# Performance work log

Measured on AMD Instinct MI355X. Metric: run time of the kernel, lower is better.

The kernel has to match this reference:

```python
import jax, jax.numpy as jnp
import numpy as np

N = 50000        # nodes
E = 800000       # edges
D_IN = 64        # input_dim
D_E = 16         # edge_dim
D_OUT = 64       # output_dim
HEADS = 8
HEAD_DIM = D_OUT // HEADS
COMB = 2 * D_IN + D_E  # 144


def _linear_init(key, fan_in, fan_out):
    kw, kb = jax.random.split(key)
    lim = 1.0 / np.sqrt(fan_in)
    W = jax.random.uniform(kw, (fan_in, fan_out), minval=-lim, maxval=lim, dtype=jnp.float32)
    b = jax.random.uniform(kb, (fan_out,), minval=-lim, maxval=lim, dtype=jnp.float32)
    return W, b


def setup_inputs() -> dict:
    key = jax.random.key(0)
    ks = jax.random.split(key, 16)
    inp = {
        "x": jax.random.normal(ks[0], (N, D_IN), dtype=jnp.float32),
        "edge_attr": jax.random.normal(ks[1], (E, D_E), dtype=jnp.float32),
        "edge_index": jax.random.randint(ks[2], (2, E), 0, N, dtype=jnp.int32),
        "q": jax.random.uniform(ks[3], (1, D_OUT), dtype=jnp.float32) * 0.1,
    }
    # three ResidualStacks: k (COMB->D_OUT), v (COMB->D_OUT), out (D_OUT->D_OUT)
    for pre, fan_in, kbase in (("k", COMB, 4), ("v", COMB, 8), ("o", D_OUT, 12)):
        W0, b0 = _linear_init(ks[kbase], fan_in, D_OUT)
        W1, b1 = _linear_init(ks[kbase + 1], D_OUT, D_OUT)
        W2, b2 = _linear_init(ks[kbase + 2], D_OUT, D_OUT)
        inp.update({f"{pre}_W0": W0, f"{pre}_b0": b0,
                    f"{pre}_W1": W1, f"{pre}_b1": b1,
                    f"{pre}_W2": W2, f"{pre}_b2": b2})
    return inp


def residual_stack(h, W0, b0, W1, b1, W2, b2, last_activation):
    # input projection + ReLU, then 2 residual linear blocks
    h = jax.nn.relu(h @ W0 + b0)
    h = jax.nn.relu(h + h @ W1 + b1)
    h = h + h @ W2 + b2
    if last_activation:
        h = jax.nn.relu(h)
    return h


def neighborhood_attention(q, k, v, index):
    # q: (1, D_OUT), k/v: (E, D_OUT), index: (E,) destination node ids
    kh = k.reshape(E, HEADS, HEAD_DIM)
    qh = q.reshape(1, HEADS, HEAD_DIM)
    scores = jnp.sum(qh * kh, axis=-1) / np.sqrt(HEAD_DIM)  # (E, HEADS)
    m = jax.ops.segment_max(scores, index, num_segments=N)  # (N, HEADS)
    ex = jnp.exp(scores - jax.lax.stop_gradient(m)[index])
    denom = jax.ops.segment_sum(ex, index, num_segments=N)  # (N, HEADS)
    alpha = ex / denom[index]
    vh = v.reshape(E, HEADS, HEAD_DIM)
    return (alpha[:, :, None] * vh).reshape(E, D_OUT)


def reference(x, edge_attr, edge_index, q,
              k_W0, k_b0, k_W1, k_b1, k_W2, k_b2,
              v_W0, v_b0, v_W1, v_b1, v_W2, v_b2,
              o_W0, o_b0, o_W1, o_b1, o_W2, o_b2):
    src, dst = edge_index[0], edge_index[1]
    feat = jnp.concatenate([x[src], x[dst], edge_attr], axis=-1)  # (E, COMB)
    k = residual_stack(feat, k_W0, k_b0, k_W1, k_b1, k_W2, k_b2, last_activation=False)
    v = residual_stack(feat, v_W0, v_b0, v_W1, v_b1, v_W2, v_b2, last_activation=False)
    messages = neighborhood_attention(q, k, v, dst)               # (E, D_OUT)
    aggr = jax.ops.segment_sum(messages, dst, num_segments=N)    # (N, D_OUT)
    out = residual_stack(jax.nn.relu(aggr), o_W0, o_b0, o_W1, o_b1, o_W2, o_b2, last_activation=False)
    # skip_connection=True, input_dim == output_dim -> identity skip
    return jax.nn.relu(x + out)
```

## Files before the change

### kernel.cpp

```cpp
#include <hip/hip_runtime.h>

#define N_NODES 50000
#define E_EDGES 800000
#define D_OUT   64
#define COMB    144

typedef float  f32x4  __attribute__((ext_vector_type(4)));
typedef __bf16 bf16x8 __attribute__((ext_vector_type(8)));
typedef __bf16 bf16x4 __attribute__((ext_vector_type(4)));

#define WS_NUM_OFF   0
#define WS_DEN_OFF   (12800000)
#define WS_WTS_OFF   (14400000)
#define BIG_ELEMS    (64*168)
#define SMALL_ELEMS  (64*72)

__global__ __launch_bounds__(256) void prep_kernel(
    const float* __restrict__ kW0, const float* __restrict__ kW1, const float* __restrict__ kW2,
    const float* __restrict__ vW0, const float* __restrict__ vW1, const float* __restrict__ vW2,
    const float* __restrict__ oW0, const float* __restrict__ oW1, const float* __restrict__ oW2,
    __bf16* __restrict__ wout)
{
    const int b = blockIdx.x, tid = threadIdx.x;
    const float* src;
    __bf16* dst;
    int K, Kpad, lb;
    if (b < 42)      { src = kW0; dst = wout;             K = 144; Kpad = 168; lb = b; }
    else if (b < 84) { src = vW0; dst = wout + BIG_ELEMS; K = 144; Kpad = 168; lb = b - 42; }
    else {
        const int id = (b - 84) / 18; lb = (b - 84) % 18;
        const float* s7[7] = {kW1, kW2, vW1, vW2, oW0, oW1, oW2};
        src = s7[id]; dst = wout + 2 * BIG_ELEMS + id * SMALL_ELEMS;
        K = 64; Kpad = 72;
    }
    const int idx = lb * 256 + tid;
    const int col = idx / Kpad, k = idx % Kpad;
    dst[idx] = (k < K) ? (__bf16)src[k * 64 + col] : (__bf16)0.f;
}

__device__ __forceinline__ void gemm64(const __bf16* Arow, const __bf16* Wt,
                                       int hi, int row16, f32x4 acc[4])
{
    #pragma unroll
    for (int kc = 0; kc < 2; ++kc) {
        const bf16x8 a = *(const bf16x8*)(Arow + kc * 32 + hi * 8);
        #pragma unroll
        for (int n = 0; n < 4; ++n) {
            const bf16x8 bfr = *(const bf16x8*)(Wt + (n * 16 + row16) * 72 + kc * 32 + hi * 8);
            acc[n] = __builtin_amdgcn_mfma_f32_16x16x32_bf16(a, bfr, acc[n], 0, 0, 0);
        }
    }
}

__global__ __launch_bounds__(256) void edge_kernel(
    const float* __restrict__ x,
    const float* __restrict__ edge_attr,
    const int*   __restrict__ edge_index,
    const float* __restrict__ q,
    const float* __restrict__ kb0, const float* __restrict__ kb1, const float* __restrict__ kb2,
    const float* __restrict__ vb0, const float* __restrict__ vb1, const float* __restrict__ vb2,
    const __bf16* __restrict__ kW0t, const __bf16* __restrict__ kW1t, const __bf16* __restrict__ kW2t,
    const __bf16* __restrict__ vW0t, const __bf16* __restrict__ vW1t, const __bf16* __restrict__ vW2t,
    float* __restrict__ num, float* __restrict__ den)
{
    __shared__ __bf16 feat_s[64][168];
    __shared__ __bf16 H0_s[64][72];
    __shared__ __bf16 H1_s[64][72];
    __shared__ int src_s[64], dst_s[64];

    const int tid  = threadIdx.x;
    const int lane = tid & 63;
    const int w    = tid >> 6;
    const int e0   = blockIdx.x * 64;
    const int row16 = lane & 15;
    const int hi    = lane >> 4;

    if (tid < 64) { src_s[tid] = edge_index[e0 + tid]; dst_s[tid] = edge_index[E_EDGES + e0 + tid]; }
    __syncthreads();

    for (int i = tid; i < 64 * 36; i += 256) {
        const int r = i / 36, j = i % 36;
        float4 f;
        if (j < 16)      f = *(const float4*)&x[(size_t)src_s[r] * 64 + j * 4];
        else if (j < 32) f = *(const float4*)&x[(size_t)dst_s[r] * 64 + (j - 16) * 4];
        else             f = *(const float4*)&edge_attr[(size_t)(e0 + r) * 16 + (j - 32) * 4];
        bf16x4 h; h[0] = (__bf16)f.x; h[1] = (__bf16)f.y; h[2] = (__bf16)f.z; h[3] = (__bf16)f.w;
        *(bf16x4*)&feat_s[r][j * 4] = h;
    }
    for (int i = tid; i < 64 * 6; i += 256) {
        bf16x4 z; z[0] = z[1] = z[2] = z[3] = (__bf16)0.f;
        *(bf16x4*)&feat_s[i / 6][144 + (i % 6) * 4] = z;
    }
    __syncthreads();

    const __bf16* frow = &feat_s[w * 16 + row16][0];
    const __bf16* hrow0 = &H0_s[w * 16 + row16][0];
    const __bf16* hrow1 = &H1_s[w * 16 + row16][0];

    float kk[4][4], vv[4][4];

    #pragma unroll
    for (int stack = 0; stack < 2; ++stack) {
        const __bf16* W0t = stack == 0 ? kW0t : vW0t;
        const __bf16* W1t = stack == 0 ? kW1t : vW1t;
        const __bf16* W2t = stack == 0 ? kW2t : vW2t;
        const float*  b0  = stack == 0 ? kb0 : vb0;
        const float*  b1  = stack == 0 ? kb1 : vb1;
        const float*  b2  = stack == 0 ? kb2 : vb2;

        f32x4 acc[4] = {{0,0,0,0},{0,0,0,0},{0,0,0,0},{0,0,0,0}};
        #pragma unroll
        for (int kc = 0; kc < 5; ++kc) {
            const bf16x8 a = *(const bf16x8*)(frow + kc * 32 + hi * 8);
            #pragma unroll
            for (int n = 0; n < 4; ++n) {
                const bf16x8 bfr = *(const bf16x8*)(W0t + (n * 16 + row16) * 168 + kc * 32 + hi * 8);
                acc[n] = __builtin_amdgcn_mfma_f32_16x16x32_bf16(a, bfr, acc[n], 0, 0, 0);
            }
        }
        float h0[4][4];
        #pragma unroll
        for (int n = 0; n < 4; ++n) {
            const float bias = b0[n * 16 + row16];
            #pragma unroll
            for (int r = 0; r < 4; ++r) {
                h0[n][r] = fmaxf(acc[n][r] + bias, 0.f);
                H0_s[w * 16 + hi * 4 + r][n * 16 + row16] = (__bf16)h0[n][r];
            }
        }

        f32x4 acc1[4] = {{0,0,0,0},{0,0,0,0},{0,0,0,0},{0,0,0,0}};
        gemm64(hrow0, W1t, hi, row16, acc1);
        float h1[4][4];
        #pragma unroll
        for (int n = 0; n < 4; ++n) {
            const float bias = b1[n * 16 + row16];
            #pragma unroll
            for (int r = 0; r < 4; ++r) {
                h1[n][r] = fmaxf(h0[n][r] + acc1[n][r] + bias, 0.f);
                H1_s[w * 16 + hi * 4 + r][n * 16 + row16] = (__bf16)h1[n][r];
            }
        }

        f32x4 acc2[4] = {{0,0,0,0},{0,0,0,0},{0,0,0,0},{0,0,0,0}};
        gemm64(hrow1, W2t, hi, row16, acc2);
        #pragma unroll
        for (int n = 0; n < 4; ++n) {
            const float bias = b2[n * 16 + row16];
            #pragma unroll
            for (int r = 0; r < 4; ++r) {
                const float o = h1[n][r] + acc2[n][r] + bias;
                if (stack == 0) kk[n][r] = o; else vv[n][r] = o;
            }
        }
    }

    float qv[4];
    #pragma unroll
    for (int n = 0; n < 4; ++n) qv[n] = q[n * 16 + row16];

    float ex[4][4];
    #pragma unroll
    for (int n = 0; n < 4; ++n)
        #pragma unroll
        for (int r = 0; r < 4; ++r) {
            float p = qv[n] * kk[n][r];
            p += __shfl_xor(p, 1);
            p += __shfl_xor(p, 2);
            p += __shfl_xor(p, 4);
            ex[n][r] = __expf(p * 0.35355339059327373f);
        }

    const int b3 = row16 >> 3;
    #pragma unroll
    for (int r = 0; r < 4; ++r) {
        const int drow = dst_s[w * 16 + hi * 4 + r];
        if ((lane & 7) == 0) {
            #pragma unroll
            for (int n = 0; n < 4; ++n)
                atomicAdd(&den[(size_t)drow * 8 + 2 * n + b3], ex[n][r]);
        }
        #pragma unroll
        for (int n = 0; n < 4; ++n)
            atomicAdd(&num[(size_t)drow * 64 + n * 16 + row16], ex[n][r] * vv[n][r]);
    }
}

__global__ __launch_bounds__(256) void node_kernel(
    const float* __restrict__ x,
    const float* __restrict__ num, const float* __restrict__ den,
    const float* __restrict__ ob0, const float* __restrict__ ob1, const float* __restrict__ ob2,
    const __bf16* __restrict__ oW0t, const __bf16* __restrict__ oW1t, const __bf16* __restrict__ oW2t,
    float* __restrict__ out)
{
    __shared__ __bf16 A_s[64][72];
    __shared__ __bf16 H0_s[64][72];
    __shared__ __bf16 H1_s[64][72];

    const int tid  = threadIdx.x;
    const int lane = tid & 63;
    const int w    = tid >> 6;
    const int n0   = blockIdx.x * 64;
    const int row16 = lane & 15;
    const int hi    = lane >> 4;

    for (int i = tid; i < 64 * 16; i += 256) {
        const int r = i >> 4, c4 = (i & 15) * 4;
        const int node = n0 + r;
        bf16x4 h; h[0] = h[1] = h[2] = h[3] = (__bf16)0.f;
        if (node < N_NODES) {
            const float dh = den[(size_t)node * 8 + (c4 >> 3)];
            if (dh > 0.f) {
                const float4 f = *(const float4*)&num[(size_t)node * 64 + c4];
                const float inv = 1.f / dh;
                h[0] = (__bf16)fmaxf(f.x * inv, 0.f);
                h[1] = (__bf16)fmaxf(f.y * inv, 0.f);
                h[2] = (__bf16)fmaxf(f.z * inv, 0.f);
                h[3] = (__bf16)fmaxf(f.w * inv, 0.f);
            }
        }
        *(bf16x4*)&A_s[r][c4] = h;
    }
    __syncthreads();

    const __bf16* arow  = &A_s[w * 16 + row16][0];
    const __bf16* hrow0 = &H0_s[w * 16 + row16][0];
    const __bf16* hrow1 = &H1_s[w * 16 + row16][0];

    f32x4 acc[4] = {{0,0,0,0},{0,0,0,0},{0,0,0,0},{0,0,0,0}};
    gemm64(arow, oW0t, hi, row16, acc);
    float h0[4][4];
    #pragma unroll
    for (int n = 0; n < 4; ++n) {
        const float bias = ob0[n * 16 + row16];
        #pragma unroll
        for (int r = 0; r < 4; ++r) {
            h0[n][r] = fmaxf(acc[n][r] + bias, 0.f);
            H0_s[w * 16 + hi * 4 + r][n * 16 + row16] = (__bf16)h0[n][r];
        }
    }

    f32x4 acc1[4] = {{0,0,0,0},{0,0,0,0},{0,0,0,0},{0,0,0,0}};
    gemm64(hrow0, oW1t, hi, row16, acc1);
    float h1[4][4];
    #pragma unroll
    for (int n = 0; n < 4; ++n) {
        const float bias = ob1[n * 16 + row16];
        #pragma unroll
        for (int r = 0; r < 4; ++r) {
            h1[n][r] = fmaxf(h0[n][r] + acc1[n][r] + bias, 0.f);
            H1_s[w * 16 + hi * 4 + r][n * 16 + row16] = (__bf16)h1[n][r];
        }
    }

    f32x4 acc2[4] = {{0,0,0,0},{0,0,0,0},{0,0,0,0},{0,0,0,0}};
    gemm64(hrow1, oW2t, hi, row16, acc2);
    #pragma unroll
    for (int n = 0; n < 4; ++n) {
        const float bias = ob2[n * 16 + row16];
        #pragma unroll
        for (int r = 0; r < 4; ++r) {
            const int node = n0 + w * 16 + hi * 4 + r;
            if (node < N_NODES) {
                const int col = n * 16 + row16;
                const float o = h1[n][r] + acc2[n][r] + bias;
                out[(size_t)node * 64 + col] = fmaxf(x[(size_t)node * 64 + col] + o, 0.f);
            }
        }
    }
}

extern "C" void kernel_launch(void* const* d_in, const int* in_sizes, int n_in,
                              void* d_out, int out_size, void* d_ws, size_t ws_size,
                              hipStream_t stream) {
    const float* x  = (const float*)d_in[0];
    const float* ea = (const float*)d_in[1];
    const int*   ei = (const int*)d_in[2];
    const float* q  = (const float*)d_in[3];
    const float* kW0 = (const float*)d_in[4];  const float* kb0 = (const float*)d_in[5];
    const float* kW1 = (const float*)d_in[6];  const float* kb1 = (const float*)d_in[7];
    const float* kW2 = (const float*)d_in[8];  const float* kb2 = (const float*)d_in[9];
    const float* vW0 = (const float*)d_in[10]; const float* vb0 = (const float*)d_in[11];
    const float* vW1 = (const float*)d_in[12]; const float* vb1 = (const float*)d_in[13];
    const float* vW2 = (const float*)d_in[14]; const float* vb2 = (const float*)d_in[15];
    const float* oW0 = (const float*)d_in[16]; const float* ob0 = (const float*)d_in[17];
    const float* oW1 = (const float*)d_in[18]; const float* ob1 = (const float*)d_in[19];
    const float* oW2 = (const float*)d_in[20]; const float* ob2 = (const float*)d_in[21];

    char* ws = (char*)d_ws;
    float*  num  = (float*)(ws + WS_NUM_OFF);
    float*  den  = (float*)(ws + WS_DEN_OFF);
    __bf16* wts  = (__bf16*)(ws + WS_WTS_OFF);
    __bf16* kW0t = wts;
    __bf16* vW0t = wts + BIG_ELEMS;
    __bf16* sm   = wts + 2 * BIG_ELEMS;
    __bf16* kW1t = sm;                  __bf16* kW2t = sm + SMALL_ELEMS;
    __bf16* vW1t = sm + 2 * SMALL_ELEMS; __bf16* vW2t = sm + 3 * SMALL_ELEMS;
    __bf16* oW0t = sm + 4 * SMALL_ELEMS; __bf16* oW1t = sm + 5 * SMALL_ELEMS;
    __bf16* oW2t = sm + 6 * SMALL_ELEMS;

    hipMemsetAsync(d_ws, 0, (size_t)N_NODES * (64 + 8) * sizeof(float), stream);

    prep_kernel<<<210, 256, 0, stream>>>(kW0, kW1, kW2, vW0, vW1, vW2, oW0, oW1, oW2, wts);

    edge_kernel<<<E_EDGES / 64, 256, 0, stream>>>(
        x, ea, ei, q,
        kb0, kb1, kb2, vb0, vb1, vb2,
        kW0t, kW1t, kW2t, vW0t, vW1t, vW2t,
        num, den);

    node_kernel<<<(N_NODES + 63) / 64, 256, 0, stream>>>(
        x, num, den, ob0, ob1, ob2, oW0t, oW1t, oW2t, (float*)d_out);
}
```

Baseline: 560.1 us.

## Make edge kernel persistent with register-prefetched gathers for next tile

The edge kernel now launches a fixed grid of 1024 blocks that loop over edge tiles with a grid stride. While the current tile's K/V MLPs run, each thread gathers the next tile's x rows and edge attributes into registers, and double-buffers the src/dst indices in shared memory. The aim is to hide gather latency behind the MFMA work and to cut block launch and setup overhead. The H0/H1 shared buffers are merged into one, and `__launch_bounds__(256,4)` caps registers, which adds pressure and a risk of spills alongside the extra prefetch registers.

```diff
diff --git a/kernel.cpp b/kernel.cpp
--- a/kernel.cpp
+++ b/kernel.cpp
@@ -4,6 +4,7 @@
 #define E_EDGES 800000
 #define D_OUT   64
 #define COMB    144
+#define GRID_E  1024
 
 typedef float  f32x4  __attribute__((ext_vector_type(4)));
 typedef __bf16 bf16x8 __attribute__((ext_vector_type(8)));
@@ -52,7 +53,7 @@
     }
 }
 
-__global__ __launch_bounds__(256) void edge_kernel(
+__global__ __launch_bounds__(256, 4) void edge_kernel(
     const float* __restrict__ x,
     const float* __restrict__ edge_attr,
     const int*   __restrict__ edge_index,
@@ -64,125 +65,226 @@
     float* __restrict__ num, float* __restrict__ den)
 {
     __shared__ __bf16 feat_s[64][168];
-    __shared__ __bf16 H0_s[64][72];
-    __shared__ __bf16 H1_s[64][72];
-    __shared__ int src_s[64], dst_s[64];
-
-    const int tid  = threadIdx.x;
-    const int lane = tid & 63;
-    const int w    = tid >> 6;
-    const int e0   = blockIdx.x * 64;
+    __shared__ __bf16 H_s[64][72];
+    __shared__ int    idx_s[2][128];
+
+    const int tid   = threadIdx.x;
+    const int lane  = tid & 63;
+    const int w     = tid >> 6;
     const int row16 = lane & 15;
     const int hi    = lane >> 4;
-
-    if (tid < 64) { src_s[tid] = edge_index[e0 + tid]; dst_s[tid] = edge_index[E_EDGES + e0 + tid]; }
-    __syncthreads();
-
-    for (int i = tid; i < 64 * 36; i += 256) {
-        const int r = i / 36, j = i % 36;
-        float4 f;
-        if (j < 16)      f = *(const float4*)&x[(size_t)src_s[r] * 64 + j * 4];
-        else if (j < 32) f = *(const float4*)&x[(size_t)dst_s[r] * 64 + (j - 16) * 4];
-        else             f = *(const float4*)&edge_attr[(size_t)(e0 + r) * 16 + (j - 32) * 4];
-        bf16x4 h; h[0] = (__bf16)f.x; h[1] = (__bf16)f.y; h[2] = (__bf16)f.z; h[3] = (__bf16)f.w;
-        *(bf16x4*)&feat_s[r][j * 4] = h;
-    }
+    const int wrow  = w * 16;
+
+    const int jj  = tid & 31;
+    const int rb  = tid >> 5;
+    const int sel = (jj < 16) ? 0 : 64;
+    const int c4  = (jj & 15) * 4;
+
+    const int nt = E_EDGES / 64;
+
     for (int i = tid; i < 64 * 6; i += 256) {
         bf16x4 z; z[0] = z[1] = z[2] = z[3] = (__bf16)0.f;
         *(bf16x4*)&feat_s[i / 6][144 + (i % 6) * 4] = z;
     }
+
+    float qv4[4];
+    #pragma unroll
+    for (int n = 0; n < 4; ++n) qv4[n] = q[n * 16 + row16];
+
+    int t = blockIdx.x;
+    if (tid < 128)
+        idx_s[0][tid] = edge_index[(tid >= 64 ? E_EDGES + t * 64 + tid - 64
+                                              : t * 64 + tid)];
     __syncthreads();
-
-    const __bf16* frow = &feat_s[w * 16 + row16][0];
-    const __bf16* hrow0 = &H0_s[w * 16 + row16][0];
-    const __bf16* hrow1 = &H1_s[w * 16 + row16][0];
-
-    float kk[4][4], vv[4][4];
-
-    #pragma unroll
-    for (int stack = 0; stack < 2; ++stack) {
-        const __bf16* W0t = stack == 0 ? kW0t : vW0t;
-        const __bf16* W1t = stack == 0 ? kW1t : vW1t;
-        const __bf16* W2t = stack == 0 ? kW2t : vW2t;
-        const float*  b0  = stack == 0 ? kb0 : vb0;
-        const float*  b1  = stack == 0 ? kb1 : vb1;
-        const float*  b2  = stack == 0 ? kb2 : vb2;
-
-        f32x4 acc[4] = {{0,0,0,0},{0,0,0,0},{0,0,0,0},{0,0,0,0}};
-        #pragma unroll
-        for (int kc = 0; kc < 5; ++kc) {
-            const bf16x8 a = *(const bf16x8*)(frow + kc * 32 + hi * 8);
-            #pragma unroll
-            for (int n = 0; n < 4; ++n) {
-                const bf16x8 bfr = *(const bf16x8*)(W0t + (n * 16 + row16) * 168 + kc * 32 + hi * 8);
-                acc[n] = __builtin_amdgcn_mfma_f32_16x16x32_bf16(a, bfr, acc[n], 0, 0, 0);
-            }
-        }
-        float h0[4][4];
-        #pragma unroll
-        for (int n = 0; n < 4; ++n) {
-            const float bias = b0[n * 16 + row16];
+    {
+        float4 g[8];
+        #pragma unroll
+        for (int k = 0; k < 8; ++k) {
+            const int node = idx_s[0][sel + rb + k * 8];
+            g[k] = *(const float4*)&x[(size_t)node * 64 + c4];
+        }
+        const float4 ea4 = *(const float4*)&edge_attr[((size_t)t * 64 + (tid >> 2)) * 16 + (tid & 3) * 4];
+        #pragma unroll
+        for (int k = 0; k < 8; ++k) {
+            bf16x4 h; h[0] = (__bf16)g[k].x; h[1] = (__bf16)g[k].y;
+                      h[2] = (__bf16)g[k].z; h[3] = (__bf16)g[k].w;
+            *(bf16x4*)&feat_s[rb + k * 8][sel + c4] = h;
+        }
+        bf16x4 he; he[0] = (__bf16)ea4.x; he[1] = (__bf16)ea4.y;
+                   he[2] = (__bf16)ea4.z; he[3] = (__bf16)ea4.w;
+        *(bf16x4*)&feat_s[tid >> 2][128 + (tid & 3) * 4] = he;
+
+        if (t + GRID_E < nt && tid < 128)
+            idx_s[1][tid] = edge_index[(tid >= 64 ? E_EDGES + (t + GRID_E) * 64 + tid - 64
+                                                  : (t + GRID_E) * 64 + tid)];
+    }
+    __syncthreads();
+
+    int bufA = 0;
+
+    for (; t < nt; t += GRID_E) {
+        const int  B    = bufA ^ 1;
+        const bool pre  = (t + GRID_E)     < nt;
+        const bool pre2 = (t + 2 * GRID_E) < nt;
+
+        float4 g[8]; float4 ea4;
+        if (pre) {
+            #pragma unroll
+            for (int k = 0; k < 8; ++k) {
+                const int node = idx_s[B][sel + rb + k * 8];
+                g[k] = *(const float4*)&x[(size_t)node * 64 + c4];
+            }
+            ea4 = *(const float4*)&edge_attr[((size_t)(t + GRID_E) * 64 + (tid >> 2)) * 16 + (tid & 3) * 4];
+        }
+        int inext = 0;
+        if (pre2 && tid < 128)
+            inext = edge_index[(tid >= 64 ? E_EDGES + (t + 2 * GRID_E) * 64 + tid - 64
+                                          : (t + 2 * GRID_E) * 64 + tid)];
+
+        const __bf16* frow = &feat_s[wrow + row16][0];
+        const __bf16* hrow = &H_s[wrow + row16][0];
+
+        float kk[4][4], vv[4][4];
+        float h0V[4][4];
+
+        {
+            f32x4 acc[4] = {{0,0,0,0},{0,0,0,0},{0,0,0,0},{0,0,0,0}};
+            #pragma unroll
+            for (int kc = 0; kc < 5; ++kc) {
+                const bf16x8 a = *(const bf16x8*)(frow + kc * 32 + hi * 8);
+                #pragma unroll
+                for (int n = 0; n < 4; ++n) {
+                    const bf16x8 bfr = *(const bf16x8*)(kW0t + (n * 16 + row16) * 168 + kc * 32 + hi * 8);
+                    acc[n] = __builtin_amdgcn_mfma_f32_16x16x32_bf16(a, bfr, acc[n], 0, 0, 0);
+                }
+            }
+            float h0[4][4];
+            #pragma unroll
+            for (int n = 0; n < 4; ++n) {
+                const float bias = kb0[n * 16 + row16];
+                #pragma unroll
+                for (int r = 0; r < 4; ++r) {
+                    h0[n][r] = fmaxf(acc[n][r] + bias, 0.f);
+                    H_s[wrow + hi * 4 + r][n * 16 + row16] = (__bf16)h0[n][r];
+                }
+            }
+            f32x4 acc1[4] = {{0,0,0,0},{0,0,0,0},{0,0,0,0},{0,0,0,0}};
+            gemm64(hrow, kW1t, hi, row16, acc1);
+            float h1[4][4];
+            #pragma unroll
+            for (int n = 0; n < 4; ++n) {
+                const float bias = kb1[n * 16 + row16];
+                #pragma unroll
+                for (int r = 0; r < 4; ++r) {
+                    h1[n][r] = fmaxf(h0[n][r] + acc1[n][r] + bias, 0.f);
+                    H_s[wrow + hi * 4 + r][n * 16 + row16] = (__bf16)h1[n][r];
+                }
+            }
+            f32x4 acc2[4] = {{0,0,0,0},{0,0,0,0},{0,0,0,0},{0,0,0,0}};
+            gemm64(hrow, kW2t, hi, row16, acc2);
+            #pragma unroll
+            for (int n = 0; n < 4; ++n) {
+                const float bias = kb2[n * 16 + row16];
+                #pragma unroll
+                for (int r = 0; r < 4; ++r)
+                    kk[n][r] = h1[n][r] + acc2[n][r] + bias;
+            }
+        }
+
+        float ex[4][4];
+        #pragma unroll
+        for (int n = 0; n < 4; ++n)
             #pragma unroll
             for (int r = 0; r < 4; ++r) {
-                h0[n][r] = fmaxf(acc[n][r] + bias, 0.f);
-                H0_s[w * 16 + hi * 4 + r][n * 16 + row16] = (__bf16)h0[n][r];
-            }
-        }
-
-        f32x4 acc1[4] = {{0,0,0,0},{0,0,0,0},{0,0,0,0},{0,0,0,0}};
-        gemm64(hrow0, W1t, hi, row16, acc1);
-        float h1[4][4];
-        #pragma unroll
-        for (int n = 0; n < 4; ++n) {
-            const float bias = b1[n * 16 + row16];
-            #pragma unroll
-            for (int r = 0; r < 4; ++r) {
-                h1[n][r] = fmaxf(h0[n][r] + acc1[n][r] + bias, 0.f);
-                H1_s[w * 16 + hi * 4 + r][n * 16 + row16] = (__bf16)h1[n][r];
-            }
-        }
-
-        f32x4 acc2[4] = {{0,0,0,0},{0,0,0,0},{0,0,0,0},{0,0,0,0}};
-        gemm64(hrow1, W2t, hi, row16, acc2);
-        #pragma unroll
-        for (int n = 0; n < 4; ++n) {
-            const float bias = b2[n * 16 + row16];
-            #pragma unroll
-            for (int r = 0; r < 4; ++r) {
-                const float o = h1[n][r] + acc2[n][r] + bias;
-                if (stack == 0) kk[n][r] = o; else vv[n][r] = o;
-            }
-        }
-    }
-
-    float qv[4];
-    #pragma unroll
-    for (int n = 0; n < 4; ++n) qv[n] = q[n * 16 + row16];
-
-    float ex[4][4];
-    #pragma unroll
-    for (int n = 0; n < 4; ++n)
+                float p = qv4[n] * kk[n][r];
+                p += __shfl_xor(p, 1);
+                p += __shfl_xor(p, 2);
+                p += __shfl_xor(p, 4);
+                ex[n][r] = __expf(p * 0.35355339059327373f);
+            }
+
+        int dst4[4];
+        #pragma unroll
+        for (int r = 0; r < 4; ++r) dst4[r] = idx_s[bufA][64 + wrow + hi * 4 + r];
+
+        {
+            f32x4 acc[4] = {{0,0,0,0},{0,0,0,0},{0,0,0,0},{0,0,0,0}};
+            #pragma unroll
+            for (int kc = 0; kc < 5; ++kc) {
+                const bf16x8 a = *(const bf16x8*)(frow + kc * 32 + hi * 8);
+                #pragma unroll
+                for (int n = 0; n < 4; ++n) {
+                    const bf16x8 bfr = *(const bf16x8*)(vW0t + (n * 16 + row16) * 168 + kc * 32 + hi * 8);
+                    acc[n] = __builtin_amdgcn_mfma_f32_16x16x32_bf16(a, bfr, acc[n], 0, 0, 0);
+                }
+            }
+            #pragma unroll
+            for (int n = 0; n < 4; ++n) {
+                const float bias = vb0[n * 16 + row16];
+                #pragma unroll
+                for (int r = 0; r < 4; ++r) {
+                    h0V[n][r] = fmaxf(acc[n][r] + bias, 0.f);
+                    H_s[wrow + hi * 4 + r][n * 16 + row16] = (__bf16)h0V[n][r];
+                }
+            }
+        }
+
+        __syncthreads();
+
+        if (pre2 && tid < 128) idx_s[bufA][tid] = inext;
+
+        {
+            f32x4 acc1[4] = {{0,0,0,0},{0,0,0,0},{0,0,0,0},{0,0,0,0}};
+            gemm64(hrow, vW1t, hi, row16, acc1);
+            float h1[4][4];
+            #pragma unroll
+            for (int n = 0; n < 4; ++n) {
+                const float bias = vb1[n * 16 + row16];
+                #pragma unroll
+                for (int r = 0; r < 4; ++r) {
+                    h1[n][r] = fmaxf(h0V[n][r] + acc1[n][r] + bias, 0.f);
+                    H_s[wrow + hi * 4 + r][n * 16 + row16] = (__bf16)h1[n][r];
+                }
+            }
+            f32x4 acc2[4] = {{0,0,0,0},{0,0,0,0},{0,0,0,0},{0,0,0,0}};
+            gemm64(hrow, vW2t, hi, row16, acc2);
+            #pragma unroll
+            for (int n = 0; n < 4; ++n) {
+                const float bias = vb2[n * 16 + row16];
+                #pragma unroll
+                for (int r = 0; r < 4; ++r)
+                    vv[n][r] = h1[n][r] + acc2[n][r] + bias;
+            }
+        }
+
+        const int b3 = row16 >> 3;
         #pragma unroll
         for (int r = 0; r < 4; ++r) {
-            float p = qv[n] * kk[n][r];
-            p += __shfl_xor(p, 1);
-            p += __shfl_xor(p, 2);
-            p += __shfl_xor(p, 4);
-            ex[n][r] = __expf(p * 0.35355339059327373f);
-        }
-
-    const int b3 = row16 >> 3;
-    #pragma unroll
-    for (int r = 0; r < 4; ++r) {
-        const int drow = dst_s[w * 16 + hi * 4 + r];
-        if ((lane & 7) == 0) {
+            const int drow = dst4[r];
+            if ((lane & 7) == 0) {
+                #pragma unroll
+                for (int n = 0; n < 4; ++n)
+                    atomicAdd(&den[(size_t)drow * 8 + 2 * n + b3], ex[n][r]);
+            }
             #pragma unroll
             for (int n = 0; n < 4; ++n)
-                atomicAdd(&den[(size_t)drow * 8 + 2 * n + b3], ex[n][r]);
-        }
-        #pragma unroll
-        for (int n = 0; n < 4; ++n)
-            atomicAdd(&num[(size_t)drow * 64 + n * 16 + row16], ex[n][r] * vv[n][r]);
+                atomicAdd(&num[(size_t)drow * 64 + n * 16 + row16], ex[n][r] * vv[n][r]);
+        }
+
+        if (pre) {
+            #pragma unroll
+            for (int k = 0; k < 8; ++k) {
+                bf16x4 h; h[0] = (__bf16)g[k].x; h[1] = (__bf16)g[k].y;
+                          h[2] = (__bf16)g[k].z; h[3] = (__bf16)g[k].w;
+                *(bf16x4*)&feat_s[rb + k * 8][sel + c4] = h;
+            }
+            bf16x4 he; he[0] = (__bf16)ea4.x; he[1] = (__bf16)ea4.y;
+                       he[2] = (__bf16)ea4.z; he[3] = (__bf16)ea4.w;
+            *(bf16x4*)&feat_s[tid >> 2][128 + (tid & 3) * 4] = he;
+        }
+
+        __syncthreads();
+        bufA ^= 1;
     }
 }
 
@@ -194,8 +296,7 @@
     float* __restrict__ out)
 {
     __shared__ __bf16 A_s[64][72];
-    __shared__ __bf16 H0_s[64][72];
-    __shared__ __bf16 H1_s[64][72];
+    __shared__ __bf16 H_s[64][72];
 
     const int tid  = threadIdx.x;
     const int lane = tid & 63;
@@ -205,13 +306,13 @@
     const int hi    = lane >> 4;
 
     for (int i = tid; i < 64 * 16; i += 256) {
-        const int r = i >> 4, c4 = (i & 15) * 4;
+        const int r = i >> 4, cc = (i & 15) * 4;
         const int node = n0 + r;
         bf16x4 h; h[0] = h[1] = h[2] = h[3] = (__bf16)0.f;
         if (node < N_NODES) {
-            const float dh = den[(size_t)node * 8 + (c4 >> 3)];
+            const float dh = den[(size_t)node * 8 + (cc >> 3)];
             if (dh > 0.f) {
-                const float4 f = *(const float4*)&num[(size_t)node * 64 + c4];
+                const float4 f = *(const float4*)&num[(size_t)node * 64 + cc];
                 const float inv = 1.f / dh;
                 h[0] = (__bf16)fmaxf(f.x * inv, 0.f);
                 h[1] = (__bf16)fmaxf(f.y * inv, 0.f);
@@ -219,13 +320,12 @@
                 h[3] = (__bf16)fmaxf(f.w * inv, 0.f);
             }
         }
-        *(bf16x4*)&A_s[r][c4] = h;
+        *(bf16x4*)&A_s[r][cc] = h;
     }
     __syncthreads();
 
-    const __bf16* arow  = &A_s[w * 16 + row16][0];
-    const __bf16* hrow0 = &H0_s[w * 16 + row16][0];
-    const __bf16* hrow1 = &H1_s[w * 16 + row16][0];
+    const __bf16* arow = &A_s[w * 16 + row16][0];
+    const __bf16* hrow = &H_s[w * 16 + row16][0];
 
     f32x4 acc[4] = {{0,0,0,0},{0,0,0,0},{0,0,0,0},{0,0,0,0}};
     gemm64(arow, oW0t, hi, row16, acc);
@@ -236,12 +336,12 @@
         #pragma unroll
         for (int r = 0; r < 4; ++r) {
             h0[n][r] = fmaxf(acc[n][r] + bias, 0.f);
-            H0_s[w * 16 + hi * 4 + r][n * 16 + row16] = (__bf16)h0[n][r];
+            H_s[w * 16 + hi * 4 + r][n * 16 + row16] = (__bf16)h0[n][r];
         }
     }
 
     f32x4 acc1[4] = {{0,0,0,0},{0,0,0,0},{0,0,0,0},{0,0,0,0}};
-    gemm64(hrow0, oW1t, hi, row16, acc1);
+    gemm64(hrow, oW1t, hi, row16, acc1);
     float h1[4][4];
     #pragma unroll
     for (int n = 0; n < 4; ++n) {
@@ -249,12 +349,12 @@
         #pragma unroll
         for (int r = 0; r < 4; ++r) {
             h1[n][r] = fmaxf(h0[n][r] + acc1[n][r] + bias, 0.f);
-            H1_s[w * 16 + hi * 4 + r][n * 16 + row16] = (__bf16)h1[n][r];
+            H_s[w * 16 + hi * 4 + r][n * 16 + row16] = (__bf16)h1[n][r];
         }
     }
 
     f32x4 acc2[4] = {{0,0,0,0},{0,0,0,0},{0,0,0,0},{0,0,0,0}};
-    gemm64(hrow1, oW2t, hi, row16, acc2);
+    gemm64(hrow, oW2t, hi, row16, acc2);
     #pragma unroll
     for (int n = 0; n < 4; ++n) {
         const float bias = ob2[n * 16 + row16];
@@ -294,7 +394,7 @@
     __bf16* kW0t = wts;
     __bf16* vW0t = wts + BIG_ELEMS;
     __bf16* sm   = wts + 2 * BIG_ELEMS;
-    __bf16* kW1t = sm;                  __bf16* kW2t = sm + SMALL_ELEMS;
+    __bf16* kW1t = sm;                   __bf16* kW2t = sm + SMALL_ELEMS;
     __bf16* vW1t = sm + 2 * SMALL_ELEMS; __bf16* vW2t = sm + 3 * SMALL_ELEMS;
     __bf16* oW0t = sm + 4 * SMALL_ELEMS; __bf16* oW1t = sm + 5 * SMALL_ELEMS;
     __bf16* oW2t = sm + 6 * SMALL_ELEMS;
@@ -303,7 +403,7 @@
 
     prep_kernel<<<210, 256, 0, stream>>>(kW0, kW1, kW2, vW0, vW1, vW2, oW0, oW1, oW2, wts);
 
-    edge_kernel<<<E_EDGES / 64, 256, 0, stream>>>(
+    edge_kernel<<<GRID_E, 256, 0, stream>>>(
         x, ea, ei, q,
         kb0, kb1, kb2, vb0, vb1, vb2,
         kW0t, kW1t, kW2t, vW0t, vW1t, vW2t,
```

After: 1.159 ms. 107% more time.
